# Kernel optimization log

Measured on AMD Instinct MI355X. Metric: run time of the kernel, lower is better.

## Reference

```python
import jax, jax.numpy as jnp
import numpy as np

N_NODES = 50000
N_EDGES = 800000
HID = 128
EDGE_DIM = 4
LAYERS = 4
MAX_Z = 100
NUM_GRAPHS = 512


def setup_inputs() -> dict:
    key = jax.random.key(0)
    ks = jax.random.split(key, 16)
    s = lambda k, shape, fan_in: jax.random.normal(k, shape, jnp.float32) / np.sqrt(fan_in)
    inp = {
        "z": jax.random.randint(ks[0], (N_NODES,), 0, MAX_Z + 1),
        "edge_index": jax.random.randint(ks[1], (2, N_EDGES), 0, N_NODES),
        "edge_attr": jax.random.normal(ks[2], (N_EDGES, EDGE_DIM), jnp.float32),
        "batch": jnp.sort(jax.random.randint(ks[3], (N_NODES,), 0, NUM_GRAPHS)),
        "emb": jax.random.normal(ks[4], (MAX_Z + 1, HID), jnp.float32),
        # stacked per-layer params; Linear stored as [in, out]
        "ew1": s(ks[5], (LAYERS, 2 * HID + EDGE_DIM, HID), 2 * HID + EDGE_DIM),
        "eb1": jnp.zeros((LAYERS, HID), jnp.float32),
        "ew2": s(ks[6], (LAYERS, HID, HID), HID),
        "eb2": jnp.zeros((LAYERS, HID), jnp.float32),
        "nw": s(ks[7], (LAYERS, 2 * HID, HID), 2 * HID),
        "nb": jnp.zeros((LAYERS, HID), jnp.float32),
        "rw1": s(ks[8], (HID, HID), HID),
        "rb1": jnp.zeros((HID,), jnp.float32),
        "rw2": s(ks[9], (HID, 1), HID),
        "rb2": jnp.zeros((1,), jnp.float32),
    }
    return inp


def _forward(z, edge_index, edge_attr, batch,
             emb, ew1, eb1, ew2, eb2, nw, nb, rw1, rb1, rw2, rb2):
    silu = jax.nn.silu
    src, dst = edge_index[0], edge_index[1]
    x = emb[z]  # [N, H]
    for l in range(LAYERS):
        m_in = jnp.concatenate([x[src], x[dst], edge_attr], axis=-1)  # [E, 2H+ed]
        h = silu(m_in @ ew1[l] + eb1[l])
        msg = silu(h @ ew2[l] + eb2[l])  # [E, H]
        agg = jax.ops.segment_sum(msg, dst, num_segments=N_NODES)  # scatter-add
        x = silu(jnp.concatenate([x, agg], axis=-1) @ nw[l] + nb[l])
    # segment mean over graphs
    sums = jax.ops.segment_sum(x, batch, num_segments=NUM_GRAPHS)
    counts = jnp.clip(jax.ops.segment_sum(jnp.ones((x.shape[0],), x.dtype), batch,
                                          num_segments=NUM_GRAPHS), 1.0)[:, None]
    g = sums / counts  # [G, H]
    pred = (silu(g @ rw1 + rb1) @ rw2 + rb2)[:, 0]  # [G]
    return pred


def reference(z, edge_index, edge_attr, batch,
              emb, ew1, eb1, ew2, eb2, nw, nb, rw1, rb1, rw2, rb2):
    return _forward(z, edge_index, edge_attr, batch,
                    emb, ew1, eb1, ew2, eb2, nw, nb, rw1, rb1, rw2, rb2)
```

## Files before the change

kernel.cpp:

```cpp
#include <hip/hip_runtime.h>
#include <math.h>

#define HID  128
#define EDIM 4

typedef unsigned short u16;
typedef u16    us8   __attribute__((ext_vector_type(8)));
typedef __bf16 bf16x8 __attribute__((ext_vector_type(8)));
typedef float  f32x4 __attribute__((ext_vector_type(4)));

__device__ __forceinline__ float silu_f(float v) {
    return v / (1.0f + __expf(-v));
}
__device__ __forceinline__ u16 f2bf(float f) {
    unsigned u = __float_as_uint(f);
    unsigned r = u + 0x7fffu + ((u >> 16) & 1u);
    return (u16)(r >> 16);
}
__device__ __forceinline__ u16 f2bf_fast(float f) {
    return (u16)((__float_as_uint(f) + 0x8000u) >> 16);
}
__device__ __forceinline__ float bf2f(u16 s) {
    return __uint_as_float(((unsigned)s) << 16);
}
__device__ __forceinline__ bf16x8 as_bf(us8 v) {
    return __builtin_bit_cast(bf16x8, v);
}

__global__ __launch_bounds__(256) void prep_wfrag(const float* __restrict__ w,
        u16* __restrict__ out, int KT, int K, int total) {
    int idx = blockIdx.x * 256 + threadIdx.x;
    if (idx >= total) return;
    int lane = idx & 63;
    int f    = (idx >> 6) % (KT * 8);
    int l    = idx / (64 * KT * 8);
    int kt = f >> 3, nt = f & 7;
    int n  = nt * 16 + (lane & 15);
    int k0 = kt * 32 + ((lane >> 4) * 8);
    us8 v;
    #pragma unroll
    for (int j = 0; j < 8; ++j) {
        int k = k0 + j;
        v[j] = (k < K) ? f2bf(w[((size_t)l * K + k) * HID + n]) : (u16)0;
    }
    *(us8*)&out[((size_t)(l * KT * 8 + f) * 64 + lane) * 8] = v;
}

__global__ __launch_bounds__(256) void hist_kernel(const int* __restrict__ dst,
        int* __restrict__ cnt, int E) {
    int e = blockIdx.x * 256 + threadIdx.x;
    if (e < E) atomicAdd(&cnt[dst[e]], 1);
}

__global__ __launch_bounds__(1024) void scan_kernel(const int* __restrict__ cnt,
        int* __restrict__ rowptr, int n) {
    __shared__ int s[1024];
    const int t = threadIdx.x;
    const int chunk = (n + 1023) >> 10;
    int lo = t * chunk, hi = lo + chunk;
    if (lo > n) lo = n;
    if (hi > n) hi = n;
    int sum = 0;
    for (int i = lo; i < hi; ++i) sum += cnt[i];
    s[t] = sum;
    __syncthreads();
    for (int off = 1; off < 1024; off <<= 1) {
        int v = (t >= off) ? s[t - off] : 0;
        __syncthreads();
        s[t] += v;
        __syncthreads();
    }
    int run = s[t] - sum;
    for (int i = lo; i < hi; ++i) { rowptr[i] = run; run += cnt[i]; }
    if (t == 1023) rowptr[n] = run;
}

__global__ __launch_bounds__(256) void scatter_kernel(const int* __restrict__ src,
        const int* __restrict__ dst, const float* __restrict__ ea,
        const int* __restrict__ rowptr, int* __restrict__ cursor,
        int* __restrict__ srcS, int* __restrict__ dstS, u16* __restrict__ eaS, int E) {
    int e = blockIdx.x * 256 + threadIdx.x;
    if (e >= E) return;
    int d = dst[e];
    int p = rowptr[d] + atomicAdd(&cursor[d], 1);
    srcS[p] = src[e];
    dstS[p] = d;
    const float* q = &ea[(size_t)e * EDIM];
    ushort4 v;
    v.x = f2bf(q[0]); v.y = f2bf(q[1]); v.z = f2bf(q[2]); v.w = f2bf(q[3]);
    *(ushort4*)&eaS[(size_t)p * 4] = v;
}

__global__ __launch_bounds__(HID) void embed_kernel(const int* __restrict__ z,
        const float* __restrict__ emb, u16* __restrict__ xb, int n) {
    int i = blockIdx.x;
    if (i >= n) return;
    int t = threadIdx.x;
    xb[(size_t)i * HID + t] = f2bf(emb[(size_t)z[i] * HID + t]);
}

__global__ __launch_bounds__(256) void edge_mfma(
        const u16* __restrict__ xin, const int* __restrict__ srcS,
        const int* __restrict__ dstS, const u16* __restrict__ eaS,
        const u16* __restrict__ w1f, const float* __restrict__ b1,
        const u16* __restrict__ w2f, const float* __restrict__ b2,
        float* __restrict__ agg, int nE) {
    __shared__ __align__(16) char smem[64 * 296 * 2];
    __shared__ int dsh[64];
    u16*   A = (u16*)smem;
    u16*   H = (u16*)smem;
    float* M = (float*)smem;

    const int t    = threadIdx.x;
    const int e0   = blockIdx.x * 64;
    const int wv   = t >> 6, lane = t & 63;
    const int lrow = lane & 15;
    const int kq   = lane >> 4;
    const int kq8  = kq * 8;
    const int rq   = kq * 4;

    #pragma unroll
    for (int it = 0; it < 8; ++it) {
        int slot = it * 256 + t;
        int row = slot >> 5, ch = slot & 31;
        int e = e0 + row; if (e >= nE) e = nE - 1;
        int node = (ch < 16) ? srcS[e] : dstS[e];
        us8 v = *(const us8*)&xin[(size_t)node * HID + (ch & 15) * 8];
        *(us8*)&A[row * 296 + ch * 8] = v;
    }
    if (t < 64) {
        int e = e0 + t;
        bool valid = e < nE; if (!valid) e = nE - 1;
        dsh[t] = valid ? dstS[e] : -1;
        ushort4 q = *(const ushort4*)&eaS[(size_t)e * 4];
        int base = t * 296 + 256;
        A[base + 0] = q.x; A[base + 1] = q.y; A[base + 2] = q.z; A[base + 3] = q.w;
        #pragma unroll
        for (int j = 4; j < 32; ++j) A[base + j] = 0;
    }
    __syncthreads();

    f32x4 acc[4][2];
    {
        float bias0 = b1[wv * 32 + lrow], bias1 = b1[wv * 32 + 16 + lrow];
        #pragma unroll
        for (int mt = 0; mt < 4; ++mt)
            #pragma unroll
            for (int r = 0; r < 4; ++r) {
                acc[mt][0][r] = bias0; acc[mt][1][r] = bias1;
            }
    }
    #pragma unroll
    for (int kt = 0; kt < 9; ++kt) {
        bf16x8 w0 = *(const bf16x8*)&w1f[((size_t)(kt * 8 + wv * 2 + 0) * 64 + lane) * 8];
        bf16x8 w1 = *(const bf16x8*)&w1f[((size_t)(kt * 8 + wv * 2 + 1) * 64 + lane) * 8];
        #pragma unroll
        for (int mt = 0; mt < 4; ++mt) {
            bf16x8 a = *(const bf16x8*)&A[(mt * 16 + lrow) * 296 + kt * 32 + kq8];
            acc[mt][0] = __builtin_amdgcn_mfma_f32_16x16x32_bf16(a, w0, acc[mt][0], 0, 0, 0);
            acc[mt][1] = __builtin_amdgcn_mfma_f32_16x16x32_bf16(a, w1, acc[mt][1], 0, 0, 0);
        }
    }
    __syncthreads();

    #pragma unroll
    for (int mt = 0; mt < 4; ++mt)
        #pragma unroll
        for (int nt2 = 0; nt2 < 2; ++nt2)
            #pragma unroll
            for (int r = 0; r < 4; ++r)
                H[(mt * 16 + rq + r) * 136 + wv * 32 + nt2 * 16 + lrow] =
                    f2bf_fast(silu_f(acc[mt][nt2][r]));
    __syncthreads();

    f32x4 acc2[4][2];
    {
        float bias0 = b2[wv * 32 + lrow], bias1 = b2[wv * 32 + 16 + lrow];
        #pragma unroll
        for (int mt = 0; mt < 4; ++mt)
            #pragma unroll
            for (int r = 0; r < 4; ++r) {
                acc2[mt][0][r] = bias0; acc2[mt][1][r] = bias1;
            }
    }
    #pragma unroll
    for (int kt = 0; kt < 4; ++kt) {
        bf16x8 w0 = *(const bf16x8*)&w2f[((size_t)(kt * 8 + wv * 2 + 0) * 64 + lane) * 8];
        bf16x8 w1 = *(const bf16x8*)&w2f[((size_t)(kt * 8 + wv * 2 + 1) * 64 + lane) * 8];
        #pragma unroll
        for (int mt = 0; mt < 4; ++mt) {
            bf16x8 a = *(const bf16x8*)&H[(mt * 16 + lrow) * 136 + kt * 32 + kq8];
            acc2[mt][0] = __builtin_amdgcn_mfma_f32_16x16x32_bf16(a, w0, acc2[mt][0], 0, 0, 0);
            acc2[mt][1] = __builtin_amdgcn_mfma_f32_16x16x32_bf16(a, w1, acc2[mt][1], 0, 0, 0);
        }
    }
    __syncthreads();

    #pragma unroll
    for (int mt = 0; mt < 4; ++mt)
        #pragma unroll
        for (int nt2 = 0; nt2 < 2; ++nt2)
            #pragma unroll
            for (int r = 0; r < 4; ++r)
                M[(mt * 16 + rq + r) * 132 + wv * 32 + nt2 * 16 + lrow] =
                    silu_f(acc2[mt][nt2][r]);
    __syncthreads();

    {
        int col = t & 127;
        int r0  = (t >> 7) * 32;
        float run = 0.f;
        int   cur = dsh[r0];
        #pragma unroll 4
        for (int i = 0; i < 32; ++i) {
            int row = r0 + i;
            run += M[row * 132 + col];
            int nxt = (i == 31) ? -2 : dsh[row + 1];
            if (cur != nxt) {
                if (cur >= 0)
                    unsafeAtomicAdd(&agg[(size_t)cur * HID + col], run);
                run = 0.f; cur = nxt;
            }
        }
    }
}

__global__ __launch_bounds__(256) void node_mfma(
        u16* __restrict__ xb, const float* __restrict__ agg,
        const u16* __restrict__ nwf, const float* __restrict__ nb, int n) {
    const int t    = threadIdx.x;
    const int i0   = blockIdx.x * 64;
    const int wv   = t >> 6, lane = t & 63;
    const int lrow = lane & 15;
    const int kq   = lane >> 4;
    const int kq8  = kq * 8;
    const int rq   = kq * 4;

    int iN[4];
    #pragma unroll
    for (int mt = 0; mt < 4; ++mt) {
        int i = i0 + mt * 16 + lrow; if (i >= n) i = n - 1;
        iN[mt] = i;
    }

    f32x4 acc[4][2];
    {
        float bias0 = nb[wv * 32 + lrow], bias1 = nb[wv * 32 + 16 + lrow];
        #pragma unroll
        for (int mt = 0; mt < 4; ++mt)
            #pragma unroll
            for (int r = 0; r < 4; ++r) {
                acc[mt][0][r] = bias0; acc[mt][1][r] = bias1;
            }
    }
    #pragma unroll
    for (int kt = 0; kt < 4; ++kt) {
        bf16x8 w0 = *(const bf16x8*)&nwf[((size_t)(kt * 8 + wv * 2 + 0) * 64 + lane) * 8];
        bf16x8 w1 = *(const bf16x8*)&nwf[((size_t)(kt * 8 + wv * 2 + 1) * 64 + lane) * 8];
        #pragma unroll
        for (int mt = 0; mt < 4; ++mt) {
            bf16x8 a = as_bf(*(const us8*)&xb[(size_t)iN[mt] * HID + kt * 32 + kq8]);
            acc[mt][0] = __builtin_amdgcn_mfma_f32_16x16x32_bf16(a, w0, acc[mt][0], 0, 0, 0);
            acc[mt][1] = __builtin_amdgcn_mfma_f32_16x16x32_bf16(a, w1, acc[mt][1], 0, 0, 0);
        }
    }
    #pragma unroll
    for (int kt = 4; kt < 8; ++kt) {
        bf16x8 w0 = *(const bf16x8*)&nwf[((size_t)(kt * 8 + wv * 2 + 0) * 64 + lane) * 8];
        bf16x8 w1 = *(const bf16x8*)&nwf[((size_t)(kt * 8 + wv * 2 + 1) * 64 + lane) * 8];
        #pragma unroll
        for (int mt = 0; mt < 4; ++mt) {
            const float* p = &agg[(size_t)iN[mt] * HID + (kt - 4) * 32 + kq8];
            float4 f0 = *(const float4*)p;
            float4 f1 = *(const float4*)(p + 4);
            us8 av;
            av[0] = f2bf_fast(f0.x); av[1] = f2bf_fast(f0.y);
            av[2] = f2bf_fast(f0.z); av[3] = f2bf_fast(f0.w);
            av[4] = f2bf_fast(f1.x); av[5] = f2bf_fast(f1.y);
            av[6] = f2bf_fast(f1.z); av[7] = f2bf_fast(f1.w);
            bf16x8 a = as_bf(av);
            acc[mt][0] = __builtin_amdgcn_mfma_f32_16x16x32_bf16(a, w0, acc[mt][0], 0, 0, 0);
            acc[mt][1] = __builtin_amdgcn_mfma_f32_16x16x32_bf16(a, w1, acc[mt][1], 0, 0, 0);
        }
    }
    __syncthreads();
    #pragma unroll
    for (int mt = 0; mt < 4; ++mt)
        #pragma unroll
        for (int nt2 = 0; nt2 < 2; ++nt2)
            #pragma unroll
            for (int r = 0; r < 4; ++r) {
                int i = i0 + mt * 16 + rq + r;
                if (i < n)
                    xb[(size_t)i * HID + wv * 32 + nt2 * 16 + lrow] =
                        f2bf_fast(silu_f(acc[mt][nt2][r]));
            }
}

__global__ __launch_bounds__(HID) void segsum_kernel(
        const u16* __restrict__ xb, const int* __restrict__ batch,
        float* __restrict__ sums, float* __restrict__ counts, int n) {
    int i = blockIdx.x;
    if (i >= n) return;
    int t = threadIdx.x;
    int b = batch[i];
    unsafeAtomicAdd(&sums[(size_t)b * HID + t], bf2f(xb[(size_t)i * HID + t]));
    if (t == 0) unsafeAtomicAdd(&counts[b], 1.0f);
}

__global__ __launch_bounds__(HID) void readout_kernel(
        const float* __restrict__ sums, const float* __restrict__ counts,
        const float* __restrict__ rw1, const float* __restrict__ rb1,
        const float* __restrict__ rw2, const float* __restrict__ rb2,
        float* __restrict__ pred) {
    __shared__ float gv[HID];
    __shared__ float hv[HID];
    const int g = blockIdx.x;
    const int t = threadIdx.x;
    float c = counts[g];
    if (c < 1.0f) c = 1.0f;
    gv[t] = sums[(size_t)g * HID + t] / c;
    __syncthreads();
    float acc = rb1[t];
    for (int k4 = 0; k4 < 32; ++k4) {
        float4 mv = *(const float4*)&gv[k4 * 4];
        #pragma unroll
        for (int j = 0; j < 4; ++j)
            acc += ((const float*)&mv)[j] * rw1[(size_t)(k4 * 4 + j) * HID + t];
    }
    hv[t] = silu_f(acc) * rw2[t];
    __syncthreads();
    for (int s = HID / 2; s > 0; s >>= 1) {
        if (t < s) hv[t] += hv[t + s];
        __syncthreads();
    }
    if (t == 0) pred[g] = hv[0] + rb2[0];
}

extern "C" void kernel_launch(void* const* d_in, const int* in_sizes, int n_in,
                              void* d_out, int out_size, void* d_ws, size_t ws_size,
                              hipStream_t stream) {
    const int*   z          = (const int*)d_in[0];
    const int*   edge_index = (const int*)d_in[1];
    const float* edge_attr  = (const float*)d_in[2];
    const int*   batch      = (const int*)d_in[3];
    const float* emb        = (const float*)d_in[4];
    const float* ew1        = (const float*)d_in[5];
    const float* eb1        = (const float*)d_in[6];
    const float* ew2        = (const float*)d_in[7];
    const float* eb2        = (const float*)d_in[8];
    const float* nw         = (const float*)d_in[9];
    const float* nb         = (const float*)d_in[10];
    const float* rw1        = (const float*)d_in[11];
    const float* rb1        = (const float*)d_in[12];
    const float* rw2        = (const float*)d_in[13];
    const float* rb2        = (const float*)d_in[14];
    float* pred = (float*)d_out;

    const int N = in_sizes[0];
    const int E = in_sizes[1] / 2;
    const int G = out_size;
    const int* srcI = edge_index;
    const int* dstI = edge_index + E;

    char* base = (char*)d_ws;
    size_t off = 0;
    auto carve = [&](size_t bytes) -> char* {
        char* p = base + off;
        off = (off + bytes + 255) & ~(size_t)255;
        return p;
    };
    float* agg    = (float*)carve((size_t)N * HID * sizeof(float));
    float* sums   = (float*)carve((size_t)G * HID * sizeof(float));
    float* cnts_g = (float*)carve((size_t)G * sizeof(float));
    u16*   xb     = (u16*)carve((size_t)N * HID * sizeof(u16));
    int*   srcS   = (int*)carve((size_t)(E + 64) * sizeof(int));
    int*   dstS   = (int*)carve((size_t)(E + 64) * sizeof(int));
    u16*   eaS    = (u16*)carve((size_t)(E + 64) * 4 * sizeof(u16));
    int*   rowptr = (int*)carve((size_t)(N + 1) * sizeof(int));
    int*   cursor = (int*)carve((size_t)N * sizeof(int));
    int*   cnt    = (int*)carve((size_t)N * sizeof(int));
    u16*   w1f    = (u16*)carve((size_t)4 * 72 * 512 * sizeof(u16));
    u16*   w2f    = (u16*)carve((size_t)4 * 32 * 512 * sizeof(u16));
    u16*   nwf    = (u16*)carve((size_t)4 * 64 * 512 * sizeof(u16));

    {
        int tot1 = 4 * 9 * 8 * 64;
        prep_wfrag<<<(tot1 + 255) / 256, 256, 0, stream>>>(ew1, w1f, 9, 2 * HID + EDIM, tot1);
        int tot2 = 4 * 4 * 8 * 64;
        prep_wfrag<<<(tot2 + 255) / 256, 256, 0, stream>>>(ew2, w2f, 4, HID, tot2);
        int tot3 = 4 * 8 * 8 * 64;
        prep_wfrag<<<(tot3 + 255) / 256, 256, 0, stream>>>(nw, nwf, 8, 2 * HID, tot3);
    }

    hipMemsetAsync(cnt,    0, (size_t)N * sizeof(int), stream);
    hipMemsetAsync(cursor, 0, (size_t)N * sizeof(int), stream);
    hist_kernel<<<(E + 255) / 256, 256, 0, stream>>>(dstI, cnt, E);
    scan_kernel<<<1, 1024, 0, stream>>>(cnt, rowptr, N);
    scatter_kernel<<<(E + 255) / 256, 256, 0, stream>>>(
        srcI, dstI, edge_attr, rowptr, cursor, srcS, dstS, eaS, E);

    embed_kernel<<<N, HID, 0, stream>>>(z, emb, xb, N);

    for (int l = 0; l < 4; ++l) {
        hipMemsetAsync(agg, 0, (size_t)N * HID * sizeof(float), stream);
        edge_mfma<<<(E + 63) / 64, 256, 0, stream>>>(
            xb, srcS, dstS, eaS,
            w1f + (size_t)l * 72 * 512, eb1 + (size_t)l * HID,
            w2f + (size_t)l * 32 * 512, eb2 + (size_t)l * HID,
            agg, E);
        node_mfma<<<(N + 63) / 64, 256, 0, stream>>>(
            xb, agg, nwf + (size_t)l * 64 * 512, nb + (size_t)l * HID, N);
    }

    hipMemsetAsync(sums,   0, (size_t)G * HID * sizeof(float), stream);
    hipMemsetAsync(cnts_g, 0, (size_t)G * sizeof(float), stream);
    segsum_kernel<<<N, HID, 0, stream>>>(xb, batch, sums, cnts_g, N);
    readout_kernel<<<G, HID, 0, stream>>>(sums, cnts_g, rw1, rb1, rw2, rb2, pred);
}
```

Baseline: 1.210 ms.

## Fuse agg zeroing and segment-sum into node kernel; swizzle edge LDS tiles

The agg buffer is now zeroed inside the embed kernel and inside node_mfma after agg has been consumed, which removes the per-layer memset. The final graph segment sum and the node counts move into the last node_mfma and the embed kernel, so the separate segsum kernel goes away. In edge_mfma the shared tiles drop their padding in favour of XOR swizzles to avoid LDS bank conflicts. The edge-attribute K-tile is loaded straight from global memory into registers, and dst indices are read from global memory instead of shared memory. Risks: extra global reads of dstS in the reduction loop, and many atomics into sums in the final layer.

```diff
diff --git a/kernel.cpp b/kernel.cpp
--- a/kernel.cpp
+++ b/kernel.cpp
@@ -92,11 +92,15 @@
 }
 
 __global__ __launch_bounds__(HID) void embed_kernel(const int* __restrict__ z,
-        const float* __restrict__ emb, u16* __restrict__ xb, int n) {
+        const float* __restrict__ emb, u16* __restrict__ xb,
+        float* __restrict__ agg, const int* __restrict__ batch,
+        float* __restrict__ counts, int n) {
     int i = blockIdx.x;
     if (i >= n) return;
     int t = threadIdx.x;
     xb[(size_t)i * HID + t] = f2bf(emb[(size_t)z[i] * HID + t]);
+    agg[(size_t)i * HID + t] = 0.f;
+    if (t == 0) unsafeAtomicAdd(&counts[batch[i]], 1.0f);
 }
 
 __global__ __launch_bounds__(256) void edge_mfma(
@@ -105,8 +109,7 @@
         const u16* __restrict__ w1f, const float* __restrict__ b1,
         const u16* __restrict__ w2f, const float* __restrict__ b2,
         float* __restrict__ agg, int nE) {
-    __shared__ __align__(16) char smem[64 * 296 * 2];
-    __shared__ int dsh[64];
+    __shared__ __align__(16) char smem[32768];
     u16*   A = (u16*)smem;
     u16*   H = (u16*)smem;
     float* M = (float*)smem;
@@ -126,17 +129,13 @@
         int e = e0 + row; if (e >= nE) e = nE - 1;
         int node = (ch < 16) ? srcS[e] : dstS[e];
         us8 v = *(const us8*)&xin[(size_t)node * HID + (ch & 15) * 8];
-        *(us8*)&A[row * 296 + ch * 8] = v;
-    }
-    if (t < 64) {
-        int e = e0 + t;
-        bool valid = e < nE; if (!valid) e = nE - 1;
-        dsh[t] = valid ? dstS[e] : -1;
-        ushort4 q = *(const ushort4*)&eaS[(size_t)e * 4];
-        int base = t * 296 + 256;
-        A[base + 0] = q.x; A[base + 1] = q.y; A[base + 2] = q.z; A[base + 3] = q.w;
-        #pragma unroll
-        for (int j = 4; j < 32; ++j) A[base + j] = 0;
+        *(us8*)&A[row * 256 + ((ch ^ (row & 7)) * 8)] = v;
+    }
+    int eIx[4];
+    #pragma unroll
+    for (int mt = 0; mt < 4; ++mt) {
+        int e = e0 + mt * 16 + lrow; if (e >= nE) e = nE - 1;
+        eIx[mt] = e;
     }
     __syncthreads();
 
@@ -151,12 +150,28 @@
             }
     }
     #pragma unroll
-    for (int kt = 0; kt < 9; ++kt) {
+    for (int kt = 0; kt < 8; ++kt) {
         bf16x8 w0 = *(const bf16x8*)&w1f[((size_t)(kt * 8 + wv * 2 + 0) * 64 + lane) * 8];
         bf16x8 w1 = *(const bf16x8*)&w1f[((size_t)(kt * 8 + wv * 2 + 1) * 64 + lane) * 8];
         #pragma unroll
         for (int mt = 0; mt < 4; ++mt) {
-            bf16x8 a = *(const bf16x8*)&A[(mt * 16 + lrow) * 296 + kt * 32 + kq8];
+            int row = mt * 16 + lrow;
+            bf16x8 a = *(const bf16x8*)&A[row * 256 + (((kt * 4 + kq) ^ (lrow & 7)) * 8)];
+            acc[mt][0] = __builtin_amdgcn_mfma_f32_16x16x32_bf16(a, w0, acc[mt][0], 0, 0, 0);
+            acc[mt][1] = __builtin_amdgcn_mfma_f32_16x16x32_bf16(a, w1, acc[mt][1], 0, 0, 0);
+        }
+    }
+    {
+        bf16x8 w0 = *(const bf16x8*)&w1f[((size_t)(8 * 8 + wv * 2 + 0) * 64 + lane) * 8];
+        bf16x8 w1 = *(const bf16x8*)&w1f[((size_t)(8 * 8 + wv * 2 + 1) * 64 + lane) * 8];
+        #pragma unroll
+        for (int mt = 0; mt < 4; ++mt) {
+            us8 av = {0, 0, 0, 0, 0, 0, 0, 0};
+            if (kq == 0) {
+                ushort4 q = *(const ushort4*)&eaS[(size_t)eIx[mt] * 4];
+                av[0] = q.x; av[1] = q.y; av[2] = q.z; av[3] = q.w;
+            }
+            bf16x8 a = as_bf(av);
             acc[mt][0] = __builtin_amdgcn_mfma_f32_16x16x32_bf16(a, w0, acc[mt][0], 0, 0, 0);
             acc[mt][1] = __builtin_amdgcn_mfma_f32_16x16x32_bf16(a, w1, acc[mt][1], 0, 0, 0);
         }
@@ -201,21 +216,29 @@
         #pragma unroll
         for (int nt2 = 0; nt2 < 2; ++nt2)
             #pragma unroll
-            for (int r = 0; r < 4; ++r)
-                M[(mt * 16 + rq + r) * 132 + wv * 32 + nt2 * 16 + lrow] =
-                    silu_f(acc2[mt][nt2][r]);
+            for (int r = 0; r < 4; ++r) {
+                int row = mt * 16 + rq + r;
+                int col = wv * 32 + nt2 * 16 + lrow;
+                M[row * 128 + (col ^ (kq << 3))] = silu_f(acc2[mt][nt2][r]);
+            }
     __syncthreads();
 
     {
         int col = t & 127;
         int r0  = (t >> 7) * 32;
+        int e   = e0 + r0;
+        int cur = (e < nE) ? dstS[e] : -1;
         float run = 0.f;
-        int   cur = dsh[r0];
         #pragma unroll 4
         for (int i = 0; i < 32; ++i) {
             int row = r0 + i;
-            run += M[row * 132 + col];
-            int nxt = (i == 31) ? -2 : dsh[row + 1];
+            run += M[row * 128 + (col ^ ((((row >> 2) & 3)) << 3))];
+            int nxt;
+            if (i == 31) nxt = -2;
+            else {
+                int e2 = e0 + row + 1;
+                nxt = (e2 < nE) ? dstS[e2] : -1;
+            }
             if (cur != nxt) {
                 if (cur >= 0)
                     unsafeAtomicAdd(&agg[(size_t)cur * HID + col], run);
@@ -226,8 +249,10 @@
 }
 
 __global__ __launch_bounds__(256) void node_mfma(
-        u16* __restrict__ xb, const float* __restrict__ agg,
-        const u16* __restrict__ nwf, const float* __restrict__ nb, int n) {
+        u16* __restrict__ xb, float* __restrict__ agg,
+        const u16* __restrict__ nwf, const float* __restrict__ nb,
+        const int* __restrict__ batch, float* __restrict__ sums,
+        int last, int n) {
     const int t    = threadIdx.x;
     const int i0   = blockIdx.x * 64;
     const int wv   = t >> 6, lane = t & 63;
@@ -283,29 +308,43 @@
             acc[mt][1] = __builtin_amdgcn_mfma_f32_16x16x32_bf16(a, w1, acc[mt][1], 0, 0, 0);
         }
     }
-    __syncthreads();
-    #pragma unroll
-    for (int mt = 0; mt < 4; ++mt)
-        #pragma unroll
-        for (int nt2 = 0; nt2 < 2; ++nt2)
-            #pragma unroll
-            for (int r = 0; r < 4; ++r) {
-                int i = i0 + mt * 16 + rq + r;
-                if (i < n)
-                    xb[(size_t)i * HID + wv * 32 + nt2 * 16 + lrow] =
-                        f2bf_fast(silu_f(acc[mt][nt2][r]));
-            }
-}
-
-__global__ __launch_bounds__(HID) void segsum_kernel(
-        const u16* __restrict__ xb, const int* __restrict__ batch,
-        float* __restrict__ sums, float* __restrict__ counts, int n) {
-    int i = blockIdx.x;
-    if (i >= n) return;
-    int t = threadIdx.x;
-    int b = batch[i];
-    unsafeAtomicAdd(&sums[(size_t)b * HID + t], bf2f(xb[(size_t)i * HID + t]));
-    if (t == 0) unsafeAtomicAdd(&counts[b], 1.0f);
+
+    if (!last) {
+        __syncthreads();
+        const float4 z4 = make_float4(0.f, 0.f, 0.f, 0.f);
+        #pragma unroll
+        for (int kt = 0; kt < 4; ++kt)
+            #pragma unroll
+            for (int mt = 0; mt < 4; ++mt) {
+                float* p = &agg[(size_t)iN[mt] * HID + kt * 32 + kq8];
+                *(float4*)p = z4; *(float4*)(p + 4) = z4;
+            }
+        #pragma unroll
+        for (int mt = 0; mt < 4; ++mt)
+            #pragma unroll
+            for (int nt2 = 0; nt2 < 2; ++nt2)
+                #pragma unroll
+                for (int r = 0; r < 4; ++r) {
+                    int i = i0 + mt * 16 + rq + r;
+                    if (i < n)
+                        xb[(size_t)i * HID + wv * 32 + nt2 * 16 + lrow] =
+                            f2bf_fast(silu_f(acc[mt][nt2][r]));
+                }
+    } else {
+        #pragma unroll
+        for (int mt = 0; mt < 4; ++mt)
+            #pragma unroll
+            for (int nt2 = 0; nt2 < 2; ++nt2)
+                #pragma unroll
+                for (int r = 0; r < 4; ++r) {
+                    int i = i0 + mt * 16 + rq + r;
+                    if (i < n) {
+                        int b = batch[i];
+                        unsafeAtomicAdd(&sums[(size_t)b * HID + wv * 32 + nt2 * 16 + lrow],
+                                        silu_f(acc[mt][nt2][r]));
+                    }
+                }
+    }
 }
 
 __global__ __launch_bounds__(HID) void readout_kernel(
@@ -395,26 +434,25 @@
 
     hipMemsetAsync(cnt,    0, (size_t)N * sizeof(int), stream);
     hipMemsetAsync(cursor, 0, (size_t)N * sizeof(int), stream);
+    hipMemsetAsync(sums,   0, (size_t)G * HID * sizeof(float), stream);
+    hipMemsetAsync(cnts_g, 0, (size_t)G * sizeof(float), stream);
     hist_kernel<<<(E + 255) / 256, 256, 0, stream>>>(dstI, cnt, E);
     scan_kernel<<<1, 1024, 0, stream>>>(cnt, rowptr, N);
     scatter_kernel<<<(E + 255) / 256, 256, 0, stream>>>(
         srcI, dstI, edge_attr, rowptr, cursor, srcS, dstS, eaS, E);
 
-    embed_kernel<<<N, HID, 0, stream>>>(z, emb, xb, N);
+    embed_kernel<<<N, HID, 0, stream>>>(z, emb, xb, agg, batch, cnts_g, N);
 
     for (int l = 0; l < 4; ++l) {
-        hipMemsetAsync(agg, 0, (size_t)N * HID * sizeof(float), stream);
         edge_mfma<<<(E + 63) / 64, 256, 0, stream>>>(
             xb, srcS, dstS, eaS,
             w1f + (size_t)l * 72 * 512, eb1 + (size_t)l * HID,
             w2f + (size_t)l * 32 * 512, eb2 + (size_t)l * HID,
             agg, E);
         node_mfma<<<(N + 63) / 64, 256, 0, stream>>>(
-            xb, agg, nwf + (size_t)l * 64 * 512, nb + (size_t)l * HID, N);
-    }
-
-    hipMemsetAsync(sums,   0, (size_t)G * HID * sizeof(float), stream);
-    hipMemsetAsync(cnts_g, 0, (size_t)G * sizeof(float), stream);
-    segsum_kernel<<<N, HID, 0, stream>>>(xb, batch, sums, cnts_g, N);
+            xb, agg, nwf + (size_t)l * 64 * 512, nb + (size_t)l * HID,
+            batch, sums, (l == 3) ? 1 : 0, N);
+    }
+
     readout_kernel<<<G, HID, 0, stream>>>(sums, cnts_g, rw1, rb1, rw2, rb2, pred);
 }
```

After: 1.427 ms. +18.0%, slower.

## Fuse agg zeroing and graph segment-sum into embed and node kernels

Applied to the files above, without the earlier changes.

Drops the per-layer memset of the agg buffer. Agg is now zeroed in embed_kernel for layer 0, and in node_mfma after each row block has been read for later layers. The final segment-sum kernel is removed: the last node_mfma atomically adds silu outputs directly into per-graph sums in fp32, and node counts are computed in embed_kernel. This saves several launches and a full pass over agg and xb, at the cost of extra writes inside node_mfma and more scattered atomics on the last layer. Zeroing agg inside node_mfma is safe only because each block writes the same rows it reads, after a barrier.

```diff
diff --git a/kernel.cpp b/kernel.cpp
--- a/kernel.cpp
+++ b/kernel.cpp
@@ -92,11 +92,15 @@
 }
 
 __global__ __launch_bounds__(HID) void embed_kernel(const int* __restrict__ z,
-        const float* __restrict__ emb, u16* __restrict__ xb, int n) {
+        const float* __restrict__ emb, u16* __restrict__ xb,
+        float* __restrict__ agg, const int* __restrict__ batch,
+        float* __restrict__ counts, int n) {
     int i = blockIdx.x;
     if (i >= n) return;
     int t = threadIdx.x;
     xb[(size_t)i * HID + t] = f2bf(emb[(size_t)z[i] * HID + t]);
+    agg[(size_t)i * HID + t] = 0.f;
+    if (t == 0) unsafeAtomicAdd(&counts[batch[i]], 1.0f);
 }
 
 __global__ __launch_bounds__(256) void edge_mfma(
@@ -226,8 +230,10 @@
 }
 
 __global__ __launch_bounds__(256) void node_mfma(
-        u16* __restrict__ xb, const float* __restrict__ agg,
-        const u16* __restrict__ nwf, const float* __restrict__ nb, int n) {
+        u16* __restrict__ xb, float* __restrict__ agg,
+        const u16* __restrict__ nwf, const float* __restrict__ nb,
+        const int* __restrict__ batch, float* __restrict__ sums,
+        int last, int n) {
     const int t    = threadIdx.x;
     const int i0   = blockIdx.x * 64;
     const int wv   = t >> 6, lane = t & 63;
@@ -283,29 +289,43 @@
             acc[mt][1] = __builtin_amdgcn_mfma_f32_16x16x32_bf16(a, w1, acc[mt][1], 0, 0, 0);
         }
     }
-    __syncthreads();
-    #pragma unroll
-    for (int mt = 0; mt < 4; ++mt)
-        #pragma unroll
-        for (int nt2 = 0; nt2 < 2; ++nt2)
-            #pragma unroll
-            for (int r = 0; r < 4; ++r) {
-                int i = i0 + mt * 16 + rq + r;
-                if (i < n)
-                    xb[(size_t)i * HID + wv * 32 + nt2 * 16 + lrow] =
-                        f2bf_fast(silu_f(acc[mt][nt2][r]));
+
+    if (!last) {
+        __syncthreads();
+        const float4 z4 = make_float4(0.f, 0.f, 0.f, 0.f);
+        #pragma unroll
+        for (int kt = 0; kt < 4; ++kt)
+            #pragma unroll
+            for (int mt = 0; mt < 4; ++mt) {
+                float* p = &agg[(size_t)iN[mt] * HID + kt * 32 + kq8];
+                *(float4*)p = z4; *(float4*)(p + 4) = z4;
             }
-}
-
-__global__ __launch_bounds__(HID) void segsum_kernel(
-        const u16* __restrict__ xb, const int* __restrict__ batch,
-        float* __restrict__ sums, float* __restrict__ counts, int n) {
-    int i = blockIdx.x;
-    if (i >= n) return;
-    int t = threadIdx.x;
-    int b = batch[i];
-    unsafeAtomicAdd(&sums[(size_t)b * HID + t], bf2f(xb[(size_t)i * HID + t]));
-    if (t == 0) unsafeAtomicAdd(&counts[b], 1.0f);
+        #pragma unroll
+        for (int mt = 0; mt < 4; ++mt)
+            #pragma unroll
+            for (int nt2 = 0; nt2 < 2; ++nt2)
+                #pragma unroll
+                for (int r = 0; r < 4; ++r) {
+                    int i = i0 + mt * 16 + rq + r;
+                    if (i < n)
+                        xb[(size_t)i * HID + wv * 32 + nt2 * 16 + lrow] =
+                            f2bf_fast(silu_f(acc[mt][nt2][r]));
+                }
+    } else {
+        #pragma unroll
+        for (int mt = 0; mt < 4; ++mt)
+            #pragma unroll
+            for (int nt2 = 0; nt2 < 2; ++nt2)
+                #pragma unroll
+                for (int r = 0; r < 4; ++r) {
+                    int i = i0 + mt * 16 + rq + r;
+                    if (i < n) {
+                        int b = batch[i];
+                        unsafeAtomicAdd(&sums[(size_t)b * HID + wv * 32 + nt2 * 16 + lrow],
+                                        silu_f(acc[mt][nt2][r]));
+                    }
+                }
+    }
 }
 
 __global__ __launch_bounds__(HID) void readout_kernel(
@@ -395,26 +415,25 @@
 
     hipMemsetAsync(cnt,    0, (size_t)N * sizeof(int), stream);
     hipMemsetAsync(cursor, 0, (size_t)N * sizeof(int), stream);
+    hipMemsetAsync(sums,   0, (size_t)G * HID * sizeof(float), stream);
+    hipMemsetAsync(cnts_g, 0, (size_t)G * sizeof(float), stream);
     hist_kernel<<<(E + 255) / 256, 256, 0, stream>>>(dstI, cnt, E);
     scan_kernel<<<1, 1024, 0, stream>>>(cnt, rowptr, N);
     scatter_kernel<<<(E + 255) / 256, 256, 0, stream>>>(
         srcI, dstI, edge_attr, rowptr, cursor, srcS, dstS, eaS, E);
 
-    embed_kernel<<<N, HID, 0, stream>>>(z, emb, xb, N);
+    embed_kernel<<<N, HID, 0, stream>>>(z, emb, xb, agg, batch, cnts_g, N);
 
     for (int l = 0; l < 4; ++l) {
-        hipMemsetAsync(agg, 0, (size_t)N * HID * sizeof(float), stream);
         edge_mfma<<<(E + 63) / 64, 256, 0, stream>>>(
             xb, srcS, dstS, eaS,
             w1f + (size_t)l * 72 * 512, eb1 + (size_t)l * HID,
             w2f + (size_t)l * 32 * 512, eb2 + (size_t)l * HID,
             agg, E);
         node_mfma<<<(N + 63) / 64, 256, 0, stream>>>(
-            xb, agg, nwf + (size_t)l * 64 * 512, nb + (size_t)l * HID, N);
-    }
-
-    hipMemsetAsync(sums,   0, (size_t)G * HID * sizeof(float), stream);
-    hipMemsetAsync(cnts_g, 0, (size_t)G * sizeof(float), stream);
-    segsum_kernel<<<N, HID, 0, stream>>>(xb, batch, sums, cnts_g, N);
+            xb, agg, nwf + (size_t)l * 64 * 512, nb + (size_t)l * HID,
+            batch, sums, (l == 3) ? 1 : 0, N);
+    }
+
     readout_kernel<<<G, HID, 0, stream>>>(sums, cnts_g, rw1, rb1, rw2, rb2, pred);
 }
```

Result: slower. 1.251 ms (+3.4%).
